# Kernel tuning notes

Measured on AMD Instinct MI355X. Metric: run time of the kernel, lower is better.

The kernel has to match this reference:

```python
import jax, jax.numpy as jnp
import numpy as np

N_NODES = 50000
N_EDGES = 800000
N_GRAPHS = 64
NEG_SLOPE = 0.2  # PyG GATConv default negative_slope


def gat_conv(x, src, dst, W, att_src, att_dst, bias, heads, out_ch, concat):
    """PyG-style GATConv (eval mode, self-loops already in src/dst)."""
    N = x.shape[0]
    h = (x @ W).reshape(N, heads, out_ch)            # [N,H,C]
    a_s = jnp.sum(h * att_src, axis=-1)              # [N,H]
    a_d = jnp.sum(h * att_dst, axis=-1)              # [N,H]
    e = jax.nn.leaky_relu(a_s[src] + a_d[dst], NEG_SLOPE)  # [E,H]
    # segment softmax over incoming edges of each dst node
    m = jax.ops.segment_max(e, dst, num_segments=N)
    m = jnp.where(jnp.isfinite(m), m, 0.0)
    ex = jnp.exp(e - m[dst])
    denom = jax.ops.segment_sum(ex, dst, num_segments=N)
    alpha = ex / (denom[dst] + 1e-16)                # [E,H]
    out = jax.ops.segment_sum(alpha[:, :, None] * h[src], dst, num_segments=N)  # [N,H,C]
    out = out.reshape(N, heads * out_ch) if concat else out.mean(axis=1)
    return out + bias


def setup_inputs() -> dict:
    key = jax.random.key(0)
    ks = jax.random.split(key, 12)
    x = jax.random.normal(ks[0], (N_NODES, 5), dtype=jnp.float32)
    edge_index = jax.random.randint(ks[1], (2, N_EDGES), 0, N_NODES, dtype=jnp.int64)
    batch = jnp.sort(jax.random.randint(ks[2], (N_NODES,), 0, N_GRAPHS, dtype=jnp.int64))
    def glorot(k, shape):
        fan_in, fan_out = shape[0], shape[-1]
        s = jnp.sqrt(6.0 / (fan_in + fan_out))
        return jax.random.uniform(k, shape, jnp.float32, -s, s)
    return {
        "x": x,
        "edge_index": edge_index,
        "batch": batch,
        "W1": glorot(ks[3], (5, 256)),
        "att_src1": glorot(ks[4], (4, 64)),
        "att_dst1": glorot(ks[5], (4, 64)),
        "b1": jnp.zeros((256,), jnp.float32),
        "W2": glorot(ks[6], (256, 64)),
        "att_src2": glorot(ks[7], (1, 64)),
        "att_dst2": glorot(ks[8], (1, 64)),
        "b2": jnp.zeros((64,), jnp.float32),
        "lin_W": glorot(ks[9], (64, 2)),
        "lin_b": jnp.zeros((2,), jnp.float32),
    }


def reference(x, edge_index, batch, W1, att_src1, att_dst1, b1,
              W2, att_src2, att_dst2, b2, lin_W, lin_b):
    N = x.shape[0]
    loops = jnp.arange(N, dtype=edge_index.dtype)
    src = jnp.concatenate([edge_index[0], loops])
    dst = jnp.concatenate([edge_index[1], loops])
    h = jax.nn.relu(gat_conv(x, src, dst, W1, att_src1, att_dst1, b1, 4, 64, True))
    h = jax.nn.relu(gat_conv(h, src, dst, W2, att_src2, att_dst2, b2, 1, 64, False))
    # global mean pool over graphs
    sums = jax.ops.segment_sum(h, batch, num_segments=N_GRAPHS)          # [G,64]
    cnts = jax.ops.segment_sum(jnp.ones((N,), h.dtype), batch, num_segments=N_GRAPHS)
    pooled = sums / jnp.maximum(cnts, 1.0)[:, None]
    return pooled @ lin_W + lin_b
```

## Files before the change

### kernel.cpp

```cpp
#include <hip/hip_runtime.h>
#include <math.h>

#define N_NODES 50000
#define N_EDGES 800000
#define N_GRAPHS 64
#define NEG_SLOPE 0.2f
#define SCAN_BS 512
#define SCAN_NB ((N_NODES + SCAN_BS - 1) / SCAN_BS)
#define N_REP 64
#define ZERO_INT4 ((N_NODES * 4 + N_REP * N_GRAPHS * 64 * 4) / 16)
#define SCAT_GRID 2048
#define NPX (N_NODES / 8)

typedef __attribute__((ext_vector_type(8))) short short8;
typedef __attribute__((ext_vector_type(4))) float f32x4;

__device__ __forceinline__ float lrelu(float x) { return x > 0.f ? x : NEG_SLOPE * x; }

__device__ __forceinline__ unsigned short f2bf(float f) {
    union { float f; unsigned int u; } v; v.f = f;
    unsigned int r = (v.u + 0x7fffu + ((v.u >> 16) & 1u)) >> 16;
    return (unsigned short)r;
}
__device__ __forceinline__ float bf2f(unsigned short b) {
    union { unsigned int u; float f; } v; v.u = ((unsigned int)b) << 16;
    return v.f;
}
__device__ __forceinline__ float bfLO(unsigned int u) {
    union { unsigned int u; float f; } v; v.u = u << 16;
    return v.f;
}
__device__ __forceinline__ float bfHI(unsigned int u) {
    union { unsigned int u; float f; } v; v.u = u & 0xffff0000u;
    return v.f;
}

__device__ __forceinline__ int lower_bound_i(const int* __restrict__ a, int n, int v) {
    int lo = 0, hi = n;
    while (lo < hi) { int m = (lo + hi) >> 1; if (a[m] < v) lo = m + 1; else hi = m; }
    return lo;
}

__global__ void k_zero(int4* __restrict__ p) {
    int i = blockIdx.x * blockDim.x + threadIdx.x;
    if (i < ZERO_INT4) p[i] = make_int4(0, 0, 0, 0);
}

__global__ void k_countrank(const int* __restrict__ dst, int* __restrict__ cnt,
                            int* __restrict__ rank) {
    const int base = (blockIdx.x * blockDim.x + threadIdx.x) * 4;
    if (base + 4 <= N_EDGES) {
        int4 d4 = *(const int4*)(dst + base);
        int4 r;
        r.x = atomicAdd(&cnt[d4.x], 1);
        r.y = atomicAdd(&cnt[d4.y], 1);
        r.z = atomicAdd(&cnt[d4.z], 1);
        r.w = atomicAdd(&cnt[d4.w], 1);
        *(int4*)(rank + base) = r;
    } else {
        for (int e = base; e < N_EDGES; ++e) rank[e] = atomicAdd(&cnt[dst[e]], 1);
    }
}

__global__ __launch_bounds__(256) void k_scatter(const int* __restrict__ src,
                                                 const int* __restrict__ dst,
                                                 const int* __restrict__ rank,
                                                 const int* __restrict__ row_start,
                                                 int* __restrict__ csr_src) {
    const int r = blockIdx.x & 7;
    const int slice = blockIdx.x >> 3;
    const int lo = r * NPX;
    const int per = (N_EDGES + (SCAT_GRID / 8) - 1) / (SCAT_GRID / 8);
    const int e0 = slice * per;
    const int e1 = min(e0 + per, N_EDGES);
    for (int e = e0 + threadIdx.x; e < e1; e += 256) {
        int d = dst[e];
        if ((unsigned)(d - lo) < (unsigned)NPX) {
            csr_src[row_start[d] + rank[e]] = src[e];
        }
    }
}

__global__ __launch_bounds__(SCAN_BS) void k_scan1(const int* __restrict__ cnt,
                                                   int* __restrict__ local_pref,
                                                   int* __restrict__ blk_sum) {
    const int t = threadIdx.x;
    const int gid = blockIdx.x * SCAN_BS + t;
    const int lane = t & 63, w = t >> 6;
    int v = (gid < N_NODES) ? cnt[gid] : 0;
    int x = v;
#pragma unroll
    for (int off = 1; off < 64; off <<= 1) {
        int y = __shfl_up(x, off, 64);
        if (lane >= off) x += y;
    }
    __shared__ int wsum[SCAN_BS / 64];
    __shared__ int wpre[SCAN_BS / 64];
    if (lane == 63) wsum[w] = x;
    __syncthreads();
    if (t == 0) {
        int run = 0;
#pragma unroll
        for (int i = 0; i < SCAN_BS / 64; ++i) { wpre[i] = run; run += wsum[i]; }
    }
    __syncthreads();
    int excl = x - v + wpre[w];
    if (gid < N_NODES) local_pref[gid] = excl;
    if (t == SCAN_BS - 1) blk_sum[blockIdx.x] = excl + v;
}

__global__ __launch_bounds__(128) void k_scan2(const int* __restrict__ blk_sum,
                                               int* __restrict__ blk_base,
                                               int* __restrict__ row_start) {
    const int t = threadIdx.x;
    const int lane = t & 63;
    int v = (t < SCAN_NB) ? blk_sum[t] : 0;
    int x = v;
#pragma unroll
    for (int off = 1; off < 64; off <<= 1) {
        int y = __shfl_up(x, off, 64);
        if (lane >= off) x += y;
    }
    __shared__ int wsum0;
    if (t == 63) wsum0 = x;
    __syncthreads();
    int excl = x - v + ((t >= 64) ? wsum0 : 0);
    if (t < SCAN_NB) blk_base[t] = excl;
    if (t == 127) row_start[N_NODES] = excl + v;
}

__global__ __launch_bounds__(SCAN_BS) void k_scan3(const int* __restrict__ local_pref,
                                                   const int* __restrict__ blk_base,
                                                   int* __restrict__ row_start) {
    const int gid = blockIdx.x * SCAN_BS + threadIdx.x;
    if (gid < N_NODES) row_start[gid] = local_pref[gid] + blk_base[blockIdx.x];
}

__global__ __launch_bounds__(256) void k_gemm1(const float* __restrict__ x,
                                               const float* __restrict__ W1,
                                               const float* __restrict__ att_s,
                                               const float* __restrict__ att_d,
                                               float4* __restrict__ a_s,
                                               float4* __restrict__ a_d) {
    __shared__ float Ws[5 * 256];
    const int t = threadIdx.x;
    for (int i = t; i < 5 * 256; i += 256) Ws[i] = W1[i];
    __syncthreads();
    const int wave = t >> 6, lane = t & 63;
    const int n = blockIdx.x * 4 + wave;
    if (n >= N_NODES) return;
    float x0 = x[n * 5 + 0], x1 = x[n * 5 + 1], x2 = x[n * 5 + 2],
          x3 = x[n * 5 + 3], x4 = x[n * 5 + 4];
    float vs[4], vd[4];
#pragma unroll
    for (int hd = 0; hd < 4; ++hd) {
        const int c = hd * 64 + lane;
        float h = x0 * Ws[c] + x1 * Ws[256 + c] + x2 * Ws[512 + c] +
                  x3 * Ws[768 + c] + x4 * Ws[1024 + c];
        vs[hd] = h * att_s[c];
        vd[hd] = h * att_d[c];
    }
#pragma unroll
    for (int off = 32; off; off >>= 1) {
#pragma unroll
        for (int hd = 0; hd < 4; ++hd) {
            vs[hd] += __shfl_xor(vs[hd], off, 64);
            vd[hd] += __shfl_xor(vd[hd], off, 64);
        }
    }
    if (lane == 0) {
        a_s[n] = make_float4(vs[0], vs[1], vs[2], vs[3]);
        a_d[n] = make_float4(vd[0], vd[1], vd[2], vd[3]);
    }
}

__global__ __launch_bounds__(256) void k_agg1(const float* __restrict__ x,
                                              const float* __restrict__ W1,
                                              const float4* __restrict__ asv,
                                              const float4* __restrict__ adv,
                                              const int* __restrict__ row_start,
                                              const int* __restrict__ csr_src,
                                              const float* __restrict__ b1,
                                              unsigned short* __restrict__ out1rm) {
    __shared__ float hand[4][4][24];
    const int t = threadIdx.x;
    const int wave = t >> 6, lane = t & 63;
    const int grp = lane >> 4, l16 = lane & 15;
    const int d = blockIdx.x * 16 + wave * 4 + grp;

    float w1r[4][5], bias[4];
#pragma unroll
    for (int h = 0; h < 4; ++h) {
#pragma unroll
        for (int i = 0; i < 5; ++i) w1r[h][i] = W1[i * 256 + h * 64 + lane];
        bias[h] = b1[h * 64 + lane];
    }

    const int beg = row_start[d], end = row_start[d + 1];
    const float4 ad = adv[d];

    float den[4] = {0.f, 0.f, 0.f, 0.f};
    float xw[4][5];
#pragma unroll
    for (int h = 0; h < 4; ++h)
#pragma unroll
        for (int i = 0; i < 5; ++i) xw[h][i] = 0.f;

    for (int cb = beg; cb < end; cb += 16) {
        const int j = cb + l16;
        if (j < end) {
            const int s = csr_src[j];
            const float4 a = asv[s];
            float w[4];
            w[0] = __expf(lrelu(a.x + ad.x));
            w[1] = __expf(lrelu(a.y + ad.y));
            w[2] = __expf(lrelu(a.z + ad.z));
            w[3] = __expf(lrelu(a.w + ad.w));
            const float* xp = x + (size_t)s * 5;
            float xv[5];
#pragma unroll
            for (int i = 0; i < 5; ++i) xv[i] = xp[i];
#pragma unroll
            for (int h = 0; h < 4; ++h) {
                den[h] += w[h];
#pragma unroll
                for (int i = 0; i < 5; ++i) xw[h][i] += w[h] * xv[i];
            }
        }
    }

#pragma unroll
    for (int off = 1; off < 16; off <<= 1) {
#pragma unroll
        for (int h = 0; h < 4; ++h) {
            den[h] += __shfl_xor(den[h], off, 64);
#pragma unroll
            for (int i = 0; i < 5; ++i) xw[h][i] += __shfl_xor(xw[h][i], off, 64);
        }
    }

    {
        const float4 as = asv[d];
        float w[4];
        w[0] = __expf(lrelu(as.x + ad.x));
        w[1] = __expf(lrelu(as.y + ad.y));
        w[2] = __expf(lrelu(as.z + ad.z));
        w[3] = __expf(lrelu(as.w + ad.w));
        const float* xp = x + (size_t)d * 5;
        float xv[5];
#pragma unroll
        for (int i = 0; i < 5; ++i) xv[i] = xp[i];
#pragma unroll
        for (int h = 0; h < 4; ++h) {
            den[h] += w[h];
#pragma unroll
            for (int i = 0; i < 5; ++i) xw[h][i] += w[h] * xv[i];
        }
    }

    if (l16 == 0) {
#pragma unroll
        for (int h = 0; h < 4; ++h) hand[wave][grp][h] = den[h];
#pragma unroll
        for (int h = 0; h < 4; ++h)
#pragma unroll
            for (int i = 0; i < 5; ++i) hand[wave][grp][4 + h * 5 + i] = xw[h][i];
    }
    __syncthreads();

#pragma unroll
    for (int n = 0; n < 4; ++n) {
        const int dn = blockIdx.x * 16 + wave * 4 + n;
        unsigned short* op = out1rm + (size_t)dn * 256;
#pragma unroll
        for (int h = 0; h < 4; ++h) {
            const float dh = hand[wave][n][h] + 1e-16f;
            float hh = hand[wave][n][4 + h * 5 + 0] * w1r[h][0]
                     + hand[wave][n][4 + h * 5 + 1] * w1r[h][1]
                     + hand[wave][n][4 + h * 5 + 2] * w1r[h][2]
                     + hand[wave][n][4 + h * 5 + 3] * w1r[h][3]
                     + hand[wave][n][4 + h * 5 + 4] * w1r[h][4];
            op[h * 64 + lane] = f2bf(fmaxf(hh / dh + bias[h], 0.f));
        }
    }
}

__global__ __launch_bounds__(256) void k_gemm2(const unsigned short* __restrict__ in,
                                               const float* __restrict__ W2,
                                               const float* __restrict__ att_s2,
                                               const float* __restrict__ att_d2,
                                               unsigned short* __restrict__ h2b,
                                               float* __restrict__ a_s2,
                                               float* __restrict__ a_d2) {
    __shared__ unsigned short lW[16384];
    const int t = threadIdx.x;
    for (int idx = t; idx < 16384; idx += 256) {
        int j = idx & 7, c16 = (idx >> 3) & 15, tt = (idx >> 7) & 3,
            g = (idx >> 9) & 3, s = idx >> 11;
        int k = 32 * s + 8 * g + j, c = 16 * tt + c16;
        lW[idx] = f2bf(W2[k * 64 + c]);
    }
    __syncthreads();
    const int wave = t >> 6, lane = t & 63;
    const int g = lane >> 4, c16 = lane & 15;
    const int nb = blockIdx.x * 64 + wave * 16;
    if (nb >= N_NODES) return;

    f32x4 acc[4];
#pragma unroll
    for (int i = 0; i < 4; ++i) acc[i] = (f32x4){0.f, 0.f, 0.f, 0.f};

    const unsigned short* arow = in + (size_t)(nb + c16) * 256;
#pragma unroll
    for (int s = 0; s < 8; ++s) {
        short8 a = *reinterpret_cast<const short8*>(arow + 32 * s + 8 * g);
#pragma unroll
        for (int tt = 0; tt < 4; ++tt) {
            short8 b = *reinterpret_cast<const short8*>(
                lW + ((((s * 4 + g) * 4 + tt) * 16 + c16) << 3));
            acc[tt] = __builtin_amdgcn_mfma_f32_16x16x32_bf16(a, b, acc[tt], 0, 0, 0);
        }
    }

    float attS[4], attD[4];
#pragma unroll
    for (int tt = 0; tt < 4; ++tt) {
        attS[tt] = att_s2[16 * tt + c16];
        attD[tt] = att_d2[16 * tt + c16];
    }
#pragma unroll
    for (int r = 0; r < 4; ++r) {
        const int node = nb + g * 4 + r;
        const bool ok = node < N_NODES;
        float vs = 0.f, vd = 0.f;
#pragma unroll
        for (int tt = 0; tt < 4; ++tt) {
            float v = acc[tt][r];
            if (ok) h2b[(size_t)node * 64 + 16 * tt + c16] = f2bf(v);
            vs += v * attS[tt];
            vd += v * attD[tt];
        }
#pragma unroll
        for (int off = 1; off < 16; off <<= 1) {
            vs += __shfl_xor(vs, off, 64);
            vd += __shfl_xor(vd, off, 64);
        }
        if (ok && c16 == 0) { a_s2[node] = vs; a_d2[node] = vd; }
    }
}

__global__ __launch_bounds__(256) void k_agg2(const unsigned int* __restrict__ h2u,
                                              const float* __restrict__ as_,
                                              const float* __restrict__ ad_,
                                              const int* __restrict__ row_start,
                                              const int* __restrict__ csr_src,
                                              const float* __restrict__ b2,
                                              const int* __restrict__ batch,
                                              float* __restrict__ sums) {
    __shared__ int2 ew[4][2][32];
    const int t = threadIdx.x;
    const int wid = t >> 6, lane = t & 63;
    const int g = lane >> 5, m = lane & 31;
    const int d = blockIdx.x * 8 + wid * 2 + g;
    const int beg = row_start[d], end = row_start[d + 1];
    const float adl = ad_[d];

    float den = 0.f, accx = 0.f, accy = 0.f;
    for (int c = beg; c < end; c += 32) {
        int rem = end - c; if (rem > 32) rem = 32;
        if (m < rem) {
            int s = csr_src[c + m];
            float w = __expf(lrelu(as_[s] + adl));
            den += w;
            ew[wid][g][m] = make_int2(s, __float_as_int(w));
        }
        int e = 0;
        for (; e + 4 <= rem; e += 4) {
            int2 p0 = ew[wid][g][e],     p1 = ew[wid][g][e + 1];
            int2 p2 = ew[wid][g][e + 2], p3 = ew[wid][g][e + 3];
            unsigned int v0 = h2u[(size_t)p0.x * 32 + m];
            unsigned int v1 = h2u[(size_t)p1.x * 32 + m];
            unsigned int v2 = h2u[(size_t)p2.x * 32 + m];
            unsigned int v3 = h2u[(size_t)p3.x * 32 + m];
            float w0 = __int_as_float(p0.y), w1 = __int_as_float(p1.y);
            float w2 = __int_as_float(p2.y), w3 = __int_as_float(p3.y);
            accx += w0 * bfLO(v0); accy += w0 * bfHI(v0);
            accx += w1 * bfLO(v1); accy += w1 * bfHI(v1);
            accx += w2 * bfLO(v2); accy += w2 * bfHI(v2);
            accx += w3 * bfLO(v3); accy += w3 * bfHI(v3);
        }
        for (; e < rem; ++e) {
            int2 p = ew[wid][g][e];
            unsigned int v = h2u[(size_t)p.x * 32 + m];
            float w = __int_as_float(p.y);
            accx += w * bfLO(v); accy += w * bfHI(v);
        }
    }
#pragma unroll
    for (int off = 16; off; off >>= 1) den += __shfl_xor(den, off, 64);
    {
        float w = __expf(lrelu(as_[d] + adl));
        den += w;
        unsigned int v = h2u[(size_t)d * 32 + m];
        accx += w * bfLO(v); accy += w * bfHI(v);
    }
    float inv = 1.0f / (den + 1e-16f);
    float v0 = fmaxf(accx * inv + b2[2 * m], 0.f);
    float v1 = fmaxf(accy * inv + b2[2 * m + 1], 0.f);
    const int rep = ((blockIdx.x << 3) + (wid << 1) + g) & (N_REP - 1);
    float* sb = sums + (size_t)rep * (N_GRAPHS * 64) + batch[d] * 64;
    atomicAdd(&sb[2 * m], v0);
    atomicAdd(&sb[2 * m + 1], v1);
}

__global__ __launch_bounds__(64) void k_final(const float* __restrict__ sums,
                                              const int* __restrict__ batch,
                                              const float* __restrict__ linW,
                                              const float* __restrict__ linb,
                                              float* __restrict__ out) {
    const int g = blockIdx.x;
    const int lane = threadIdx.x;
    float s = 0.f;
#pragma unroll 8
    for (int r = 0; r < N_REP; ++r)
        s += sums[(size_t)r * (N_GRAPHS * 64) + g * 64 + lane];
    int beg = lower_bound_i(batch, N_NODES, g);
    int end = lower_bound_i(batch, N_NODES, g + 1);
    float val = s / fmaxf((float)(end - beg), 1.0f);
    float v0 = val * linW[lane * 2 + 0];
    float v1 = val * linW[lane * 2 + 1];
#pragma unroll
    for (int off = 32; off; off >>= 1) {
        v0 += __shfl_xor(v0, off, 64);
        v1 += __shfl_xor(v1, off, 64);
    }
    if (lane == 0) {
        out[g * 2 + 0] = v0 + linb[0];
        out[g * 2 + 1] = v1 + linb[1];
    }
}

extern "C" void kernel_launch(void* const* d_in, const int* in_sizes, int n_in,
                              void* d_out, int out_size, void* d_ws, size_t ws_size,
                              hipStream_t stream) {
    const float* x    = (const float*)d_in[0];
    const int*   ei   = (const int*)d_in[1];
    const int*   bat  = (const int*)d_in[2];
    const float* W1   = (const float*)d_in[3];
    const float* as1  = (const float*)d_in[4];
    const float* ad1  = (const float*)d_in[5];
    const float* b1   = (const float*)d_in[6];
    const float* W2   = (const float*)d_in[7];
    const float* as2  = (const float*)d_in[8];
    const float* ad2  = (const float*)d_in[9];
    const float* b2   = (const float*)d_in[10];
    const float* linW = (const float*)d_in[11];
    const float* linb = (const float*)d_in[12];
    float* out = (float*)d_out;

    const int* src = ei;
    const int* dst = ei + N_EDGES;

    char* w = (char*)d_ws;
    unsigned short* out1rm = (unsigned short*)w; w += (size_t)N_NODES * 256 * 2;
    float4* a_s1 = (float4*)w; w += (size_t)N_NODES * 16;
    float4* a_d1 = (float4*)w; w += (size_t)N_NODES * 16;
    unsigned short* h2b = (unsigned short*)w; w += (size_t)N_NODES * 64 * 2;
    float* a_s2  = (float*)w; w += (size_t)N_NODES * 4;
    float* a_d2  = (float*)w; w += (size_t)N_NODES * 4;
    int* counts  = (int*)w;   w += (size_t)N_NODES * 4;
    float* sums  = (float*)w; w += (size_t)N_REP * N_GRAPHS * 64 * 4;
    int* row_start = (int*)w; w += (size_t)(N_NODES + 64) * 4;
    int* lpref     = (int*)w; w += (size_t)N_NODES * 4;
    int* rank      = (int*)w; w += (size_t)N_EDGES * 4;
    int* csr_src   = (int*)w; w += (size_t)N_EDGES * 4;
    int* blk_sum   = (int*)w; w += 128 * 4;
    int* blk_base  = (int*)w; w += 128 * 4;

    k_zero<<<(ZERO_INT4 + 255) / 256, 256, 0, stream>>>((int4*)counts);
    k_countrank<<<(N_EDGES / 4 + 255) / 256, 256, 0, stream>>>(dst, counts, rank);
    k_scan1<<<SCAN_NB, SCAN_BS, 0, stream>>>(counts, lpref, blk_sum);
    k_scan2<<<1, 128, 0, stream>>>(blk_sum, blk_base, row_start);
    k_scan3<<<SCAN_NB, SCAN_BS, 0, stream>>>(lpref, blk_base, row_start);
    k_scatter<<<SCAT_GRID, 256, 0, stream>>>(src, dst, rank, row_start, csr_src);

    k_gemm1<<<(N_NODES + 3) / 4, 256, 0, stream>>>(x, W1, as1, ad1, a_s1, a_d1);
    k_agg1<<<N_NODES / 16, 256, 0, stream>>>(x, W1, a_s1, a_d1, row_start, csr_src, b1, out1rm);
    k_gemm2<<<(N_NODES + 63) / 64, 256, 0, stream>>>(out1rm, W2, as2, ad2, h2b, a_s2, a_d2);
    k_agg2<<<N_NODES / 8, 256, 0, stream>>>((const unsigned int*)h2b, a_s2, a_d2,
                                            row_start, csr_src, b2, bat, sums);
    k_final<<<N_GRAPHS, 64, 0, stream>>>(sums, bat, linW, linb, out);
}
```

Before: 205.8 us.

## Pad node features to float4 and vectorize layer-2 gather to 16-byte rows

Measured after the change: 378.8 us. 1.84x slower.

```diff
diff --git a/kernel.cpp b/kernel.cpp
--- a/kernel.cpp
+++ b/kernel.cpp
@@ -44,6 +44,15 @@
 __global__ void k_zero(int4* __restrict__ p) {
     int i = blockIdx.x * blockDim.x + threadIdx.x;
     if (i < ZERO_INT4) p[i] = make_int4(0, 0, 0, 0);
+}
+
+__global__ void k_xpad(const float* __restrict__ x, float4* __restrict__ xp4) {
+    int n = blockIdx.x * blockDim.x + threadIdx.x;
+    if (n < N_NODES) {
+        const float* p = x + (size_t)n * 5;
+        xp4[n * 2]     = make_float4(p[0], p[1], p[2], p[3]);
+        xp4[n * 2 + 1] = make_float4(p[4], 0.f, 0.f, 0.f);
+    }
 }
 
 __global__ void k_countrank(const int* __restrict__ dst, int* __restrict__ cnt,
@@ -174,7 +183,7 @@
     }
 }
 
-__global__ __launch_bounds__(256) void k_agg1(const float* __restrict__ x,
+__global__ __launch_bounds__(256) void k_agg1(const float4* __restrict__ xp4,
                                               const float* __restrict__ W1,
                                               const float4* __restrict__ asv,
                                               const float4* __restrict__ adv,
@@ -216,10 +225,9 @@
             w[1] = __expf(lrelu(a.y + ad.y));
             w[2] = __expf(lrelu(a.z + ad.z));
             w[3] = __expf(lrelu(a.w + ad.w));
-            const float* xp = x + (size_t)s * 5;
-            float xv[5];
-#pragma unroll
-            for (int i = 0; i < 5; ++i) xv[i] = xp[i];
+            float4 xa = xp4[2 * s];
+            float4 xb = xp4[2 * s + 1];
+            float xv[5] = {xa.x, xa.y, xa.z, xa.w, xb.x};
 #pragma unroll
             for (int h = 0; h < 4; ++h) {
                 den[h] += w[h];
@@ -246,10 +254,9 @@
         w[1] = __expf(lrelu(as.y + ad.y));
         w[2] = __expf(lrelu(as.z + ad.z));
         w[3] = __expf(lrelu(as.w + ad.w));
-        const float* xp = x + (size_t)d * 5;
-        float xv[5];
-#pragma unroll
-        for (int i = 0; i < 5; ++i) xv[i] = xp[i];
+        float4 xa = xp4[2 * d];
+        float4 xb = xp4[2 * d + 1];
+        float xv[5] = {xa.x, xa.y, xa.z, xa.w, xb.x};
 #pragma unroll
         for (int h = 0; h < 4; ++h) {
             den[h] += w[h];
@@ -349,7 +356,7 @@
     }
 }
 
-__global__ __launch_bounds__(256) void k_agg2(const unsigned int* __restrict__ h2u,
+__global__ __launch_bounds__(256) void k_agg2(const uint4* __restrict__ h2q,
                                               const float* __restrict__ as_,
                                               const float* __restrict__ ad_,
                                               const int* __restrict__ row_start,
@@ -357,60 +364,71 @@
                                               const float* __restrict__ b2,
                                               const int* __restrict__ batch,
                                               float* __restrict__ sums) {
-    __shared__ int2 ew[4][2][32];
+    __shared__ int2 ew[4][64];
     const int t = threadIdx.x;
     const int wid = t >> 6, lane = t & 63;
-    const int g = lane >> 5, m = lane & 31;
-    const int d = blockIdx.x * 8 + wid * 2 + g;
+    const int es = lane >> 3, q = lane & 7;
+    const int d = blockIdx.x * 4 + wid;
     const int beg = row_start[d], end = row_start[d + 1];
     const float adl = ad_[d];
 
-    float den = 0.f, accx = 0.f, accy = 0.f;
-    for (int c = beg; c < end; c += 32) {
-        int rem = end - c; if (rem > 32) rem = 32;
-        if (m < rem) {
-            int s = csr_src[c + m];
+    float acc[8];
+#pragma unroll
+    for (int k = 0; k < 8; ++k) acc[k] = 0.f;
+    float den = 0.f;
+
+    for (int c = beg; c < end; c += 64) {
+        int rem = end - c; if (rem > 64) rem = 64;
+        if (lane < rem) {
+            int s = csr_src[c + lane];
             float w = __expf(lrelu(as_[s] + adl));
             den += w;
-            ew[wid][g][m] = make_int2(s, __float_as_int(w));
-        }
-        int e = 0;
-        for (; e + 4 <= rem; e += 4) {
-            int2 p0 = ew[wid][g][e],     p1 = ew[wid][g][e + 1];
-            int2 p2 = ew[wid][g][e + 2], p3 = ew[wid][g][e + 3];
-            unsigned int v0 = h2u[(size_t)p0.x * 32 + m];
-            unsigned int v1 = h2u[(size_t)p1.x * 32 + m];
-            unsigned int v2 = h2u[(size_t)p2.x * 32 + m];
-            unsigned int v3 = h2u[(size_t)p3.x * 32 + m];
-            float w0 = __int_as_float(p0.y), w1 = __int_as_float(p1.y);
-            float w2 = __int_as_float(p2.y), w3 = __int_as_float(p3.y);
-            accx += w0 * bfLO(v0); accy += w0 * bfHI(v0);
-            accx += w1 * bfLO(v1); accy += w1 * bfHI(v1);
-            accx += w2 * bfLO(v2); accy += w2 * bfHI(v2);
-            accx += w3 * bfLO(v3); accy += w3 * bfHI(v3);
-        }
-        for (; e < rem; ++e) {
-            int2 p = ew[wid][g][e];
-            unsigned int v = h2u[(size_t)p.x * 32 + m];
+            ew[wid][lane] = make_int2(s, __float_as_int(w));
+        }
+        const int nb8 = (rem + 7) >> 3;
+#pragma unroll 2
+        for (int it = 0; it < nb8; ++it) {
+            int i = it * 8 + es;
+            int2 p = (i < rem) ? ew[wid][i] : make_int2(0, 0);
             float w = __int_as_float(p.y);
-            accx += w * bfLO(v); accy += w * bfHI(v);
-        }
-    }
-#pragma unroll
-    for (int off = 16; off; off >>= 1) den += __shfl_xor(den, off, 64);
+            uint4 v = h2q[(size_t)p.x * 8 + q];
+            acc[0] += w * bfLO(v.x); acc[1] += w * bfHI(v.x);
+            acc[2] += w * bfLO(v.y); acc[3] += w * bfHI(v.y);
+            acc[4] += w * bfLO(v.z); acc[5] += w * bfHI(v.z);
+            acc[6] += w * bfLO(v.w); acc[7] += w * bfHI(v.w);
+        }
+    }
+
     {
         float w = __expf(lrelu(as_[d] + adl));
-        den += w;
-        unsigned int v = h2u[(size_t)d * 32 + m];
-        accx += w * bfLO(v); accy += w * bfHI(v);
-    }
-    float inv = 1.0f / (den + 1e-16f);
-    float v0 = fmaxf(accx * inv + b2[2 * m], 0.f);
-    float v1 = fmaxf(accy * inv + b2[2 * m + 1], 0.f);
-    const int rep = ((blockIdx.x << 3) + (wid << 1) + g) & (N_REP - 1);
-    float* sb = sums + (size_t)rep * (N_GRAPHS * 64) + batch[d] * 64;
-    atomicAdd(&sb[2 * m], v0);
-    atomicAdd(&sb[2 * m + 1], v1);
+        if (es == 0) {
+            uint4 v = h2q[(size_t)d * 8 + q];
+            acc[0] += w * bfLO(v.x); acc[1] += w * bfHI(v.x);
+            acc[2] += w * bfLO(v.y); acc[3] += w * bfHI(v.y);
+            acc[4] += w * bfLO(v.z); acc[5] += w * bfHI(v.z);
+            acc[6] += w * bfLO(v.w); acc[7] += w * bfHI(v.w);
+        }
+        if (lane == 0) den += w;
+    }
+
+#pragma unroll
+    for (int off = 8; off < 64; off <<= 1) {
+#pragma unroll
+        for (int k = 0; k < 8; ++k) acc[k] += __shfl_xor(acc[k], off, 64);
+    }
+#pragma unroll
+    for (int off = 1; off < 64; off <<= 1) den += __shfl_xor(den, off, 64);
+
+    if (es == 0) {
+        float inv = 1.0f / (den + 1e-16f);
+        const int rep = d & (N_REP - 1);
+        float* sb = sums + (size_t)rep * (N_GRAPHS * 64) + batch[d] * 64 + q * 8;
+#pragma unroll
+        for (int k = 0; k < 8; ++k) {
+            float v = fmaxf(acc[k] * inv + b2[q * 8 + k], 0.f);
+            atomicAdd(&sb[k], v);
+        }
+    }
 }
 
 __global__ __launch_bounds__(64) void k_final(const float* __restrict__ sums,
@@ -474,10 +492,12 @@
     int* lpref     = (int*)w; w += (size_t)N_NODES * 4;
     int* rank      = (int*)w; w += (size_t)N_EDGES * 4;
     int* csr_src   = (int*)w; w += (size_t)N_EDGES * 4;
+    float4* xp4    = (float4*)w; w += (size_t)N_NODES * 32;
     int* blk_sum   = (int*)w; w += 128 * 4;
     int* blk_base  = (int*)w; w += 128 * 4;
 
     k_zero<<<(ZERO_INT4 + 255) / 256, 256, 0, stream>>>((int4*)counts);
+    k_xpad<<<(N_NODES + 255) / 256, 256, 0, stream>>>(x, xp4);
     k_countrank<<<(N_EDGES / 4 + 255) / 256, 256, 0, stream>>>(dst, counts, rank);
     k_scan1<<<SCAN_NB, SCAN_BS, 0, stream>>>(counts, lpref, blk_sum);
     k_scan2<<<1, 128, 0, stream>>>(blk_sum, blk_base, row_start);
@@ -485,9 +505,9 @@
     k_scatter<<<SCAT_GRID, 256, 0, stream>>>(src, dst, rank, row_start, csr_src);
 
     k_gemm1<<<(N_NODES + 3) / 4, 256, 0, stream>>>(x, W1, as1, ad1, a_s1, a_d1);
-    k_agg1<<<N_NODES / 16, 256, 0, stream>>>(x, W1, a_s1, a_d1, row_start, csr_src, b1, out1rm);
+    k_agg1<<<N_NODES / 16, 256, 0, stream>>>(xp4, W1, a_s1, a_d1, row_start, csr_src, b1, out1rm);
     k_gemm2<<<(N_NODES + 63) / 64, 256, 0, stream>>>(out1rm, W2, as2, ad2, h2b, a_s2, a_d2);
-    k_agg2<<<N_NODES / 8, 256, 0, stream>>>((const unsigned int*)h2b, a_s2, a_d2,
+    k_agg2<<<N_NODES / 4, 256, 0, stream>>>((const uint4*)h2b, a_s2, a_d2,
                                             row_start, csr_src, b2, bat, sums);
     k_final<<<N_GRAPHS, 64, 0, stream>>>(sums, bat, linW, linb, out);
 }
```
